# Optimization experiments

Hardware: AMD Instinct MI355X
Metric: run time of the kernel (lower is better)

The kernel has to match this reference:

```python
import jax, jax.numpy as jnp
import numpy as np
import math

D_MODEL = 2048
N_HEADS = 16
D_HEAD = D_MODEL // N_HEADS
SCALE = 1.0 / math.sqrt(D_HEAD)


def setup_inputs() -> dict:
    key = jax.random.key(0)
    kx, kq, kk, kv, ko = jax.random.split(key, 5)
    x = jax.random.normal(kx, (2, 2048, D_MODEL), dtype=jnp.float32)
    W_q = jax.random.normal(kq, (D_MODEL, D_MODEL), dtype=jnp.float32)
    W_k = jax.random.normal(kk, (D_MODEL, D_MODEL), dtype=jnp.float32)
    W_v = jax.random.normal(kv, (D_MODEL, D_MODEL), dtype=jnp.float32) * math.sqrt(2.0 / D_MODEL)
    W_o = jax.random.normal(ko, (D_MODEL, D_MODEL), dtype=jnp.float32) * math.sqrt(2.0 / D_MODEL)
    return {"x": x, "W_q": W_q, "W_k": W_k, "W_v": W_v, "W_o": W_o}


def reference(x, W_q, W_k, W_v, W_o) -> jnp.ndarray:
    B, S, D = x.shape
    q = (x @ W_q).reshape(B, S, N_HEADS, D_HEAD)  # [b, q, h, dh]
    k = (x @ W_k).reshape(B, S, N_HEADS, D_HEAD)  # [b, k, h, dh]
    v = x @ W_v                                    # [b, k, d_model] (NOT split into heads)
    scores = jnp.einsum('bqhd,bkhd->bhqk', q, k)   # [b, h, q, k]
    # Faithful quirk: additive -1e9 causal mask applied BEFORE the scale.
    mask = jnp.triu(jnp.full((S, S), -1e9, dtype=scores.dtype), k=1)
    scores = (scores + mask) * SCALE
    probs = jax.nn.softmax(scores, axis=-1)
    # Faithful quirk: sums over heads h AND keys k against full-width v.
    out = jnp.einsum('bhqk,bkd->bqd', probs, v)    # [b, q, d_model]
    return out @ W_o
```

## Files before the change

### kernel.cpp

```cpp
#include <hip/hip_runtime.h>

typedef unsigned short u16;
typedef __attribute__((ext_vector_type(8))) short bf16x8;
typedef __attribute__((ext_vector_type(4))) float f32x4;

#define DEV __device__ __forceinline__
#define EXP2(x) __builtin_amdgcn_exp2f(x)
#define LOG2(x) __builtin_amdgcn_logf(x)

DEV u16 f2bf(float f) {
  union { float f; unsigned u; } v; v.f = f;
  unsigned r = v.u + 0x7fffu + ((v.u >> 16) & 1u);
  return (u16)(r >> 16);
}
DEV float bf2f(u16 h) {
  union { unsigned u; float f; } v; v.u = ((unsigned)h) << 16;
  return v.f;
}
DEV f32x4 mfma16(bf16x8 a, bf16x8 b, f32x4 c) {
  return __builtin_amdgcn_mfma_f32_16x16x32_bf16(a, b, c, 0, 0, 0);
}
DEV void cp16(const u16* g, u16* l) {
  __builtin_amdgcn_global_load_lds((__attribute__((address_space(1))) void*)g,
                                   (__attribute__((address_space(3))) void*)l, 16, 0, 0);
}

__global__ __launch_bounds__(256) void split_pair(const float4* __restrict__ x,
                                                  u16* __restrict__ hi, u16* __restrict__ lo) {
  const size_t i = (size_t)blockIdx.x * 256 + threadIdx.x;
  const float4 v = x[i];
  ushort4 h, l;
  h.x = f2bf(v.x); l.x = f2bf(v.x - bf2f(h.x));
  h.y = f2bf(v.y); l.y = f2bf(v.y - bf2f(h.y));
  h.z = f2bf(v.z); l.z = f2bf(v.z - bf2f(h.z));
  h.w = f2bf(v.w); l.w = f2bf(v.w - bf2f(h.w));
  *(ushort4*)&hi[i * 4] = h;
  *(ushort4*)&lo[i * 4] = l;
}

template<bool LO>
__global__ __launch_bounds__(256) void transpose_split(const float* __restrict__ W,
                                                       u16* __restrict__ Th, u16* __restrict__ Tl) {
  __shared__ float t[64][65];
  const int r0 = blockIdx.y * 64, c0 = blockIdx.x * 64;
  const int rr = threadIdx.x >> 4, c4 = (threadIdx.x & 15) * 4;
#pragma unroll
  for (int p = 0; p < 4; ++p) {
    const float4 v = *(const float4*)&W[(size_t)(r0 + p * 16 + rr) * 2048 + c0 + c4];
    t[p * 16 + rr][c4 + 0] = v.x; t[p * 16 + rr][c4 + 1] = v.y;
    t[p * 16 + rr][c4 + 2] = v.z; t[p * 16 + rr][c4 + 3] = v.w;
  }
  __syncthreads();
#pragma unroll
  for (int p = 0; p < 4; ++p) {
    const int cc = p * 16 + rr;
    const float v0 = t[c4 + 0][cc], v1 = t[c4 + 1][cc], v2 = t[c4 + 2][cc], v3 = t[c4 + 3][cc];
    ushort4 h;
    h.x = f2bf(v0); h.y = f2bf(v1); h.z = f2bf(v2); h.w = f2bf(v3);
    *(ushort4*)&Th[(size_t)(c0 + cc) * 2048 + r0 + c4] = h;
    if constexpr (LO) {
      ushort4 l;
      l.x = f2bf(v0 - bf2f(h.x)); l.y = f2bf(v1 - bf2f(h.y));
      l.z = f2bf(v2 - bf2f(h.z)); l.w = f2bf(v3 - bf2f(h.w));
      *(ushort4*)&Tl[(size_t)(c0 + cc) * 2048 + r0 + c4] = l;
    }
  }
}

template<bool SPLIT3, int OUTMODE, bool KLIM>
__global__ __launch_bounds__(256, 2) void gemm_bt(
    const u16* __restrict__ Aph, const u16* __restrict__ Apl,
    const u16* __restrict__ Bph, const u16* __restrict__ Bpl,
    const u16* __restrict__ Bph2, const u16* __restrict__ Bpl2,
    void* __restrict__ C0, void* __restrict__ C1,
    void* __restrict__ C0b, void* __restrict__ C1b,
    const int M, const int N, const int K, const int bShift) {
  extern __shared__ u16 lds[];
  constexpr int T_AL = 4096;
  constexpr int T_BH = SPLIT3 ? 8192 : 4096;
  constexpr int T_BL = 12288;
  if (blockIdx.z) { Bph = Bph2; Bpl = Bpl2; C0 = C0b; C1 = C1b; }
  const int tid = threadIdx.x;
  const int wave = tid >> 6, lane = tid & 63;
  const int li = lane & 15, l4 = lane >> 4;
  const int m0 = blockIdx.y * 128, n0 = blockIdx.x * 128;
  const int wr = (wave >> 1) * 64, wc = (wave & 1) * 64;
  const u16* Bh = Bph; const u16* Bl = Bpl;
  if (bShift) { const size_t s = (size_t)(m0 >> 11) * (size_t)bShift; Bh += s; if (SPLIT3) Bl += s; }

  const f32x4 fz = {0.f, 0.f, 0.f, 0.f};
  f32x4 acc[4][4];
#pragma unroll
  for (int m = 0; m < 4; ++m)
#pragma unroll
    for (int n = 0; n < 4; ++n) acc[m][n] = fz;

  const size_t aoff = (size_t)(m0 + (tid >> 2)) * K + (tid & 3) * 8;
  const size_t boff = (size_t)(n0 + (tid >> 2)) * K + (tid & 3) * 8;
  const size_t rstep = (size_t)64 * K;
  const int s0 = tid * 8, s1 = 2048 + tid * 8;
  const int abase = (wr + li) * 32 + l4 * 8;
  const int bbase = (wc + li) * 32 + l4 * 8;
  const int kEnd = KLIM ? ((m0 & 2047) + 128 < K ? (m0 & 2047) + 128 : K) : K;

#pragma unroll 1
  for (int k0 = 0; k0 < kEnd; k0 += 32) {
    cp16(Aph + aoff + k0,         &lds[s0]);
    cp16(Aph + aoff + rstep + k0, &lds[s1]);
    cp16(Bh + boff + k0,          &lds[T_BH + s0]);
    cp16(Bh + boff + rstep + k0,  &lds[T_BH + s1]);
    if constexpr (SPLIT3) {
      cp16(Apl + aoff + k0,         &lds[T_AL + s0]);
      cp16(Apl + aoff + rstep + k0, &lds[T_AL + s1]);
      cp16(Bl + boff + k0,          &lds[T_BL + s0]);
      cp16(Bl + boff + rstep + k0,  &lds[T_BL + s1]);
    }
    __syncthreads();
    bf16x8 af[4], bf_[4];
#pragma unroll
    for (int m = 0; m < 4; ++m) af[m] = *(const bf16x8*)&lds[abase + m * 512];
#pragma unroll
    for (int n = 0; n < 4; ++n) bf_[n] = *(const bf16x8*)&lds[T_BH + bbase + n * 512];
    if constexpr (SPLIT3) {
      bf16x8 alf[4], blf[4];
#pragma unroll
      for (int m = 0; m < 4; ++m) alf[m] = *(const bf16x8*)&lds[T_AL + abase + m * 512];
#pragma unroll
      for (int n = 0; n < 4; ++n) blf[n] = *(const bf16x8*)&lds[T_BL + bbase + n * 512];
#pragma unroll
      for (int m = 0; m < 4; ++m)
#pragma unroll
        for (int n = 0; n < 4; ++n) {
          acc[m][n] = mfma16(af[m], bf_[n], acc[m][n]);
          acc[m][n] = mfma16(af[m], blf[n], acc[m][n]);
          acc[m][n] = mfma16(alf[m], bf_[n], acc[m][n]);
        }
    } else {
#pragma unroll
      for (int m = 0; m < 4; ++m)
#pragma unroll
        for (int n = 0; n < 4; ++n)
          acc[m][n] = mfma16(af[m], bf_[n], acc[m][n]);
    }
    __syncthreads();
  }

#pragma unroll
  for (int m = 0; m < 4; ++m) {
#pragma unroll
    for (int n = 0; n < 4; ++n) {
      const int rg0 = m0 + wr + m * 16 + l4 * 4;
      const int cg  = n0 + wc + n * 16 + li;
      if constexpr (OUTMODE == 0) {
        u16* Ch = (u16*)C0; u16* Cl = (u16*)C1;
#pragma unroll
        for (int r = 0; r < 4; ++r) {
          const float v = acc[m][n][r];
          const u16 h = f2bf(v);
          Ch[(size_t)(rg0 + r) * N + cg] = h;
          Cl[(size_t)(rg0 + r) * N + cg] = f2bf(v - bf2f(h));
        }
      } else if constexpr (OUTMODE == 1) {
        u16* Cs = (u16*)C0;
#pragma unroll
        for (int r = 0; r < 4; ++r) Cs[(size_t)(rg0 + r) * N + cg] = f2bf(acc[m][n][r]);
      } else if constexpr (OUTMODE == 2) {
        u16* Vt = (u16*)C0;
        ushort4 pk;
        pk.x = f2bf(acc[m][n][0]); pk.y = f2bf(acc[m][n][1]);
        pk.z = f2bf(acc[m][n][2]); pk.w = f2bf(acc[m][n][3]);
        *(ushort4*)&Vt[(size_t)(rg0 >> 11) * 4194304 + (size_t)cg * 2048 + (rg0 & 2047)] = pk;
      } else {
        float* Cf = (float*)C0;
#pragma unroll
        for (int r = 0; r < 4; ++r) Cf[(size_t)(rg0 + r) * N + cg] = acc[m][n][r];
      }
    }
  }
}

#define C2EXP 0.1275174381027786f

__global__ __launch_bounds__(256) void attn_lse_part(
    const u16* __restrict__ Qh, const u16* __restrict__ Ql,
    const u16* __restrict__ Kh, const u16* __restrict__ Kl,
    float* __restrict__ Mp, float* __restrict__ Lp) {
  const int j = blockIdx.x, qt = 15 - (int)blockIdx.y, hb = blockIdx.z;
  const int b = hb >> 4, h = hb & 15;
  const int tid = threadIdx.x;
  const int nch = (2 * qt + 5) >> 2;
  if (j >= nch) {
    if (tid < 128) {
      const size_t o = ((size_t)hb * 8 + j) * 2048 + qt * 128 + tid;
      Mp[o] = -3.0e38f; Lp[o] = 0.f;
    }
    return;
  }
  __shared__ __align__(16) u16 kb[16384];
  const int wave = tid >> 6, lane = tid & 63;
  const int li = lane & 15, l4 = lane >> 4;
  const int q0w = qt * 128 + wave * 32;
  const int rs = ((li << 6) | (l4 << 4)) ^ (((li >> 1) & 7) << 4);

  bf16x8 qfh[2][4], qfl[2][4];
#pragma unroll
  for (int mf = 0; mf < 2; ++mf) {
    const size_t qo = ((size_t)(b * 2048 + q0w + mf * 16 + li)) * 2048 + h * 128 + l4 * 8;
#pragma unroll
    for (int ks = 0; ks < 4; ++ks) {
      qfh[mf][ks] = *(const bf16x8*)&Qh[qo + ks * 32];
      qfl[mf][ks] = *(const bf16x8*)&Ql[qo + ks * 32];
    }
  }
  float m[2][4], l[2][4];
#pragma unroll
  for (int mf = 0; mf < 2; ++mf)
#pragma unroll
    for (int r = 0; r < 4; ++r) { m[mf][r] = -3.0e38f; l[mf][r] = 0.f; }

  const int kst = 4 * j;
  const int ken = min(4 * j + 4, 2 * qt + 2);
  const size_t kgbase = ((size_t)b * 2048) * 2048 + h * 128;
  const f32x4 fz = {0.f, 0.f, 0.f, 0.f};

#pragma unroll 1
  for (int t = kst; t < ken; ++t) {
    __syncthreads();
#pragma unroll
    for (int i = 0; i < 4; ++i) {
      const int o = (tid + i * 256) * 16;
      const int op = o ^ (((o >> 7) & 7) << 4);
      const int dck = op >> 12, s = (op >> 6) & 63, dl = (op >> 1) & 31;
      const size_t g = kgbase + (size_t)(t * 64 + s) * 2048 + dck * 32 + dl;
      cp16(Kh + g, kb + (o >> 1));
      cp16(Kl + g, kb + 8192 + (o >> 1));
    }
    __syncthreads();

    f32x4 av0[4], av1[4];
#pragma unroll
    for (int sn = 0; sn < 4; ++sn) {
      if (64 * t + 16 * sn <= q0w + 31) {
        f32x4 a0 = fz, a1 = fz;
#pragma unroll
        for (int ks = 0; ks < 4; ++ks) {
          const bf16x8 kh = *(const bf16x8*)((const char*)kb + ks * 4096 + (sn << 10) + rs);
          const bf16x8 kl = *(const bf16x8*)((const char*)kb + 16384 + ks * 4096 + (sn << 10) + rs);
          a0 = mfma16(qfh[0][ks], kh, a0);
          a0 = mfma16(qfh[0][ks], kl, a0);
          a0 = mfma16(qfl[0][ks], kh, a0);
          a1 = mfma16(qfh[1][ks], kh, a1);
          a1 = mfma16(qfh[1][ks], kl, a1);
          a1 = mfma16(qfl[1][ks], kh, a1);
        }
        av0[sn] = a0; av1[sn] = a1;
      }
    }
#pragma unroll
    for (int r = 0; r < 4; ++r) {
      float mx0 = m[0][r], mx1 = m[1][r];
      float am0[4], am1[4];
#pragma unroll
      for (int sn = 0; sn < 4; ++sn) {
        if (64 * t + 16 * sn <= q0w + 31) {
          const int kg = t * 64 + sn * 16 + li;
          am0[sn] = (kg <= q0w + l4 * 4 + r)      ? av0[sn][r] : -3.0e38f;
          am1[sn] = (kg <= q0w + 16 + l4 * 4 + r) ? av1[sn][r] : -3.0e38f;
          mx0 = fmaxf(mx0, am0[sn]);
          mx1 = fmaxf(mx1, am1[sn]);
        }
      }
      float s0 = 0.f, s1 = 0.f;
#pragma unroll
      for (int sn = 0; sn < 4; ++sn) {
        if (64 * t + 16 * sn <= q0w + 31) {
          s0 += EXP2((am0[sn] - mx0) * C2EXP);
          s1 += EXP2((am1[sn] - mx1) * C2EXP);
        }
      }
      l[0][r] = l[0][r] * EXP2((m[0][r] - mx0) * C2EXP) + s0;
      l[1][r] = l[1][r] * EXP2((m[1][r] - mx1) * C2EXP) + s1;
      m[0][r] = mx0; m[1][r] = mx1;
    }
  }
#pragma unroll
  for (int off = 1; off <= 8; off <<= 1) {
#pragma unroll
    for (int mf = 0; mf < 2; ++mf)
#pragma unroll
      for (int r = 0; r < 4; ++r) {
        const float om = __shfl_xor(m[mf][r], off, 64);
        const float ol = __shfl_xor(l[mf][r], off, 64);
        const float mn = fmaxf(m[mf][r], om);
        l[mf][r] = l[mf][r] * EXP2((m[mf][r] - mn) * C2EXP) + ol * EXP2((om - mn) * C2EXP);
        m[mf][r] = mn;
      }
  }
  if (li == 0) {
#pragma unroll
    for (int mf = 0; mf < 2; ++mf)
#pragma unroll
      for (int r = 0; r < 4; ++r) {
        const size_t o = ((size_t)hb * 8 + j) * 2048 + q0w + mf * 16 + l4 * 4 + r;
        Mp[o] = m[mf][r];
        Lp[o] = l[mf][r];
      }
  }
}

__global__ __launch_bounds__(256) void attn_lse_merge(
    const float* __restrict__ Mp, const float* __restrict__ Lp, float* __restrict__ LSE) {
  const int id = blockIdx.x * 256 + threadIdx.x;
  const int q = id & 2047, hb = id >> 11;
  const size_t base = (size_t)hb * 8 * 2048 + q;
  float m = Mp[base], l = Lp[base];
#pragma unroll
  for (int jj = 1; jj < 8; ++jj) {
    const float om = Mp[base + jj * 2048];
    const float ol = Lp[base + jj * 2048];
    const float mn = fmaxf(m, om);
    l = l * EXP2((m - mn) * C2EXP) + ol * EXP2((om - mn) * C2EXP);
    m = mn;
  }
  LSE[(size_t)hb * 2048 + q] = m * C2EXP + LOG2(l);
}

__global__ __launch_bounds__(256) void attn_psum(
    const u16* __restrict__ Qh, const u16* __restrict__ Ql,
    const u16* __restrict__ Kh, const u16* __restrict__ Kl,
    const float* __restrict__ LSE, u16* __restrict__ Psum) {
  const int kt = blockIdx.x, qt = blockIdx.y, b = blockIdx.z;
  const int q0 = qt * 128, k0 = kt * 64;
  const int tid = threadIdx.x;

  if (k0 > q0 + 127) {
    const size_t o = ((size_t)(b * 2048 + q0 + (tid >> 1))) * 2048 + k0 + (tid & 1) * 32;
    const uint4 z = {0u, 0u, 0u, 0u};
#pragma unroll
    for (int j2 = 0; j2 < 4; ++j2) *(uint4*)&Psum[o + j2 * 8] = z;
    return;
  }

  __shared__ __align__(16) u16 kb[16384];
  const int wave = tid >> 6, lane = tid & 63;
  const int li = lane & 15, l4 = lane >> 4;
  const int q0w = q0 + wave * 32;
  const int rs = ((li << 6) | (l4 << 4)) ^ (((li >> 1) & 7) << 4);
  int snmax = ((q0w + 31 - k0) >> 4) + 1;
  snmax = snmax < 0 ? 0 : (snmax > 4 ? 4 : snmax);

  const f32x4 fz = {0.f, 0.f, 0.f, 0.f};
  f32x4 ps[2][4];
#pragma unroll
  for (int mf = 0; mf < 2; ++mf)
#pragma unroll
    for (int sn = 0; sn < 4; ++sn) ps[mf][sn] = fz;

  const size_t kgbase = ((size_t)(b * 2048 + k0)) * 2048;
  const size_t qbase0 = ((size_t)(b * 2048 + q0w + li)) * 2048 + l4 * 8;
  const size_t qbase1 = qbase0 + (size_t)16 * 2048;
  const size_t lbase  = (size_t)(b * 16) * 2048 + q0w + l4 * 4;

#pragma unroll 1
  for (int h = 0; h < 16; ++h) {
    __syncthreads();
#pragma unroll
    for (int i = 0; i < 4; ++i) {
      const int o = (tid + i * 256) * 16;
      const int op = o ^ (((o >> 7) & 7) << 4);
      const int dck = op >> 12, s = (op >> 6) & 63, dl = (op >> 1) & 31;
      const size_t g = kgbase + (size_t)s * 2048 + h * 128 + dck * 32 + dl;
      cp16(Kh + g, kb + (o >> 1));
      cp16(Kl + g, kb + 8192 + (o >> 1));
    }
    bf16x8 qfh0[4], qfl0[4], qfh1[4], qfl1[4];
    float clse[2][4];
#pragma unroll
    for (int ks = 0; ks < 4; ++ks) {
      qfh0[ks] = *(const bf16x8*)&Qh[qbase0 + (size_t)h * 128 + ks * 32];
      qfl0[ks] = *(const bf16x8*)&Ql[qbase0 + (size_t)h * 128 + ks * 32];
      qfh1[ks] = *(const bf16x8*)&Qh[qbase1 + (size_t)h * 128 + ks * 32];
      qfl1[ks] = *(const bf16x8*)&Ql[qbase1 + (size_t)h * 128 + ks * 32];
    }
#pragma unroll
    for (int mf = 0; mf < 2; ++mf)
#pragma unroll
      for (int r = 0; r < 4; ++r)
        clse[mf][r] = LSE[lbase + (size_t)h * 2048 + mf * 16 + r];
    __syncthreads();

#pragma unroll
    for (int sn = 0; sn < 4; ++sn) {
      if (sn < snmax) {
        f32x4 a0 = fz, a1 = fz;
#pragma unroll
        for (int ks = 0; ks < 4; ++ks) {
          const bf16x8 kh = *(const bf16x8*)((const char*)kb + ks * 4096 + (sn << 10) + rs);
          const bf16x8 kl = *(const bf16x8*)((const char*)kb + 16384 + ks * 4096 + (sn << 10) + rs);
          a0 = mfma16(qfh0[ks], kh, a0);
          a0 = mfma16(qfh0[ks], kl, a0);
          a0 = mfma16(qfl0[ks], kh, a0);
          a1 = mfma16(qfh1[ks], kh, a1);
          a1 = mfma16(qfh1[ks], kl, a1);
          a1 = mfma16(qfl1[ks], kh, a1);
        }
        const int kg = k0 + sn * 16 + li;
#pragma unroll
        for (int r = 0; r < 4; ++r) {
          if (kg <= q0w + l4 * 4 + r)      ps[0][sn][r] += EXP2(a0[r] * C2EXP - clse[0][r]);
          if (kg <= q0w + 16 + l4 * 4 + r) ps[1][sn][r] += EXP2(a1[r] * C2EXP - clse[1][r]);
        }
      }
    }
  }

#pragma unroll
  for (int mf = 0; mf < 2; ++mf)
#pragma unroll
    for (int sn = 0; sn < 4; ++sn) {
      const size_t o0 = ((size_t)(b * 2048 + q0w + mf * 16 + l4 * 4)) * 2048 + k0 + sn * 16 + li;
#pragma unroll
      for (int r = 0; r < 4; ++r) Psum[o0 + (size_t)r * 2048] = f2bf(ps[mf][sn][r]);
    }
}

extern "C" void kernel_launch(void* const* d_in, const int* in_sizes, int n_in,
                              void* d_out, int out_size, void* d_ws, size_t ws_size,
                              hipStream_t stream) {
  (void)in_sizes; (void)n_in; (void)out_size; (void)ws_size;
  const float* x  = (const float*)d_in[0];
  const float* Wq = (const float*)d_in[1];
  const float* Wk = (const float*)d_in[2];
  const float* Wv = (const float*)d_in[3];
  const float* Wo = (const float*)d_in[4];
  u16* ws = (u16*)d_ws;
  const size_t E8 = 8388608, E4 = 4194304;
  u16* xh = ws;
  u16* xl = ws + E8;
  u16* Qh = ws + 2 * E8;
  u16* Ql = ws + 3 * E8;
  u16* Kh = ws + 4 * E8;
  u16* Kl = ws + 5 * E8;
  u16* Vt = ws + 6 * E8;
  u16* WTh = ws + 7 * E8;
  u16* WTl = ws + 7 * E8 + E4;
  u16* WTb = ws + 7 * E8 + 2 * E4;
  u16* WkTh = Vt;
  u16* WkTl = Vt + E4;
  float* LSEf = (float*)WTl;
  float* Mp   = LSEf + 65536;
  float* Lp   = Mp + 524288;
  u16* Psum = xl;
  u16* out1 = xh;

  split_pair<<<8192, 256, 0, stream>>>((const float4*)x, xh, xl);

  dim3 tg(32, 32);

  transpose_split<true ><<<tg, 256, 0, stream>>>(Wq, WTh, WTl);
  transpose_split<true ><<<tg, 256, 0, stream>>>(Wk, WkTh, WkTl);
  transpose_split<false><<<tg, 256, 0, stream>>>(Wv, WTb, nullptr);

  gemm_bt<true, 0, false><<<dim3(16, 32, 2), 256, 32768, stream>>>(
      xh, xl, WTh, WTl, WkTh, WkTl, Qh, Ql, Kh, Kl, 4096, 2048, 2048, 0);

  gemm_bt<false, 2, false><<<dim3(16, 32), 256, 16384, stream>>>(
      xh, nullptr, WTb, nullptr, nullptr, nullptr, Vt, nullptr, nullptr, nullptr,
      4096, 2048, 2048, 0);

  attn_lse_part<<<dim3(8, 16, 32), 256, 0, stream>>>(Qh, Ql, Kh, Kl, Mp, Lp);
  attn_lse_merge<<<256, 256, 0, stream>>>(Mp, Lp, LSEf);
  attn_psum<<<dim3(32, 16, 2), 256, 0, stream>>>(Qh, Ql, Kh, Kl, LSEf, Psum);

  gemm_bt<false, 1, true><<<dim3(16, 32), 256, 16384, stream>>>(
      Psum, nullptr, Vt, nullptr, nullptr, nullptr, out1, nullptr, nullptr, nullptr,
      4096, 2048, 2048, 4194304);

  transpose_split<false><<<tg, 256, 0, stream>>>(Wo, WTb, nullptr);
  gemm_bt<false, 3, false><<<dim3(16, 32), 256, 16384, stream>>>(
      out1, nullptr, WTb, nullptr, nullptr, nullptr, d_out, nullptr, nullptr, nullptr,
      4096, 2048, 2048, 0);
}
```

Baseline: 704.1 us.

## Use lazy-rescale online LSE, halve key splits, and XCD-swizzle GEMM tiles

The LSE partial kernel now updates each running max and sum element by element. It rescales only when a score exceeds the current max by a threshold, which avoids the per-tile max pass and most rescale exponentials. Key chunks per block double (8 tiles instead of 4), so partials and the merge loop shrink from 8 to 4 splits, giving fewer blocks and less partial traffic. GEMM tile indices are remapped so consecutive block IDs spread across the XCDs, which groups M tiles for L2 reuse. The threshold approach lets the unscaled sum grow large, up to about 2^8 per element, which carries some overflow and precision risk. The longer per-block chains reduce parallelism for causal rows.

```diff
diff --git a/kernel.cpp b/kernel.cpp
--- a/kernel.cpp
+++ b/kernel.cpp
@@ -83,7 +83,10 @@
   const int tid = threadIdx.x;
   const int wave = tid >> 6, lane = tid & 63;
   const int li = lane & 15, l4 = lane >> 4;
-  const int m0 = blockIdx.y * 128, n0 = blockIdx.x * 128;
+  const int lin0 = ((int)blockIdx.y << 4) | (int)blockIdx.x;
+  const int xcd = lin0 & 7, idx = lin0 >> 3;
+  const int m0 = ((xcd << 2) | (idx & 3)) * 128;
+  const int n0 = (idx >> 2) * 128;
   const int wr = (wave >> 1) * 64, wc = (wave & 1) * 64;
   const u16* Bh = Bph; const u16* Bl = Bpl;
   if (bShift) { const size_t s = (size_t)(m0 >> 11) * (size_t)bShift; Bh += s; if (SPLIT3) Bl += s; }
@@ -180,6 +183,7 @@
 }
 
 #define C2EXP 0.1275174381027786f
+#define DMTHR 62.73f
 
 __global__ __launch_bounds__(256) void attn_lse_part(
     const u16* __restrict__ Qh, const u16* __restrict__ Ql,
@@ -188,10 +192,10 @@
   const int j = blockIdx.x, qt = 15 - (int)blockIdx.y, hb = blockIdx.z;
   const int b = hb >> 4, h = hb & 15;
   const int tid = threadIdx.x;
-  const int nch = (2 * qt + 5) >> 2;
+  const int nch = (qt >> 2) + 1;
   if (j >= nch) {
     if (tid < 128) {
-      const size_t o = ((size_t)hb * 8 + j) * 2048 + qt * 128 + tid;
+      const size_t o = ((size_t)hb * 4 + j) * 2048 + qt * 128 + tid;
       Mp[o] = -3.0e38f; Lp[o] = 0.f;
     }
     return;
@@ -218,8 +222,8 @@
 #pragma unroll
     for (int r = 0; r < 4; ++r) { m[mf][r] = -3.0e38f; l[mf][r] = 0.f; }
 
-  const int kst = 4 * j;
-  const int ken = min(4 * j + 4, 2 * qt + 2);
+  const int kst = j * 8;
+  const int ken = min(j * 8 + 8, qt * 2 + 2);
   const size_t kgbase = ((size_t)b * 2048) * 2048 + h * 128;
   const f32x4 fz = {0.f, 0.f, 0.f, 0.f};
 
@@ -236,8 +240,6 @@
       cp16(Kl + g, kb + 8192 + (o >> 1));
     }
     __syncthreads();
-
-    f32x4 av0[4], av1[4];
 #pragma unroll
     for (int sn = 0; sn < 4; ++sn) {
       if (64 * t + 16 * sn <= q0w + 31) {
@@ -253,34 +255,21 @@
           a1 = mfma16(qfh[1][ks], kl, a1);
           a1 = mfma16(qfl[1][ks], kh, a1);
         }
-        av0[sn] = a0; av1[sn] = a1;
+        const int kg = t * 64 + sn * 16 + li;
+#pragma unroll
+        for (int r = 0; r < 4; ++r) {
+          if (kg <= q0w + l4 * 4 + r) {
+            const float d = a0[r] - m[0][r];
+            if (d > DMTHR) { l[0][r] = l[0][r] * EXP2(-d * C2EXP) + 1.f; m[0][r] = a0[r]; }
+            else           { l[0][r] += EXP2(d * C2EXP); }
+          }
+          if (kg <= q0w + 16 + l4 * 4 + r) {
+            const float d = a1[r] - m[1][r];
+            if (d > DMTHR) { l[1][r] = l[1][r] * EXP2(-d * C2EXP) + 1.f; m[1][r] = a1[r]; }
+            else           { l[1][r] += EXP2(d * C2EXP); }
+          }
+        }
       }
-    }
-#pragma unroll
-    for (int r = 0; r < 4; ++r) {
-      float mx0 = m[0][r], mx1 = m[1][r];
-      float am0[4], am1[4];
-#pragma unroll
-      for (int sn = 0; sn < 4; ++sn) {
-        if (64 * t + 16 * sn <= q0w + 31) {
-          const int kg = t * 64 + sn * 16 + li;
-          am0[sn] = (kg <= q0w + l4 * 4 + r)      ? av0[sn][r] : -3.0e38f;
-          am1[sn] = (kg <= q0w + 16 + l4 * 4 + r) ? av1[sn][r] : -3.0e38f;
-          mx0 = fmaxf(mx0, am0[sn]);
-          mx1 = fmaxf(mx1, am1[sn]);
-        }
-      }
-      float s0 = 0.f, s1 = 0.f;
-#pragma unroll
-      for (int sn = 0; sn < 4; ++sn) {
-        if (64 * t + 16 * sn <= q0w + 31) {
-          s0 += EXP2((am0[sn] - mx0) * C2EXP);
-          s1 += EXP2((am1[sn] - mx1) * C2EXP);
-        }
-      }
-      l[0][r] = l[0][r] * EXP2((m[0][r] - mx0) * C2EXP) + s0;
-      l[1][r] = l[1][r] * EXP2((m[1][r] - mx1) * C2EXP) + s1;
-      m[0][r] = mx0; m[1][r] = mx1;
     }
   }
 #pragma unroll
@@ -301,7 +290,7 @@
     for (int mf = 0; mf < 2; ++mf)
 #pragma unroll
       for (int r = 0; r < 4; ++r) {
-        const size_t o = ((size_t)hb * 8 + j) * 2048 + q0w + mf * 16 + l4 * 4 + r;
+        const size_t o = ((size_t)hb * 4 + j) * 2048 + q0w + mf * 16 + l4 * 4 + r;
         Mp[o] = m[mf][r];
         Lp[o] = l[mf][r];
       }
@@ -312,10 +301,10 @@
     const float* __restrict__ Mp, const float* __restrict__ Lp, float* __restrict__ LSE) {
   const int id = blockIdx.x * 256 + threadIdx.x;
   const int q = id & 2047, hb = id >> 11;
-  const size_t base = (size_t)hb * 8 * 2048 + q;
+  const size_t base = (size_t)hb * 4 * 2048 + q;
   float m = Mp[base], l = Lp[base];
 #pragma unroll
-  for (int jj = 1; jj < 8; ++jj) {
+  for (int jj = 1; jj < 4; ++jj) {
     const float om = Mp[base + jj * 2048];
     const float ol = Lp[base + jj * 2048];
     const float mn = fmaxf(m, om);
@@ -449,7 +438,7 @@
   u16* WkTl = Vt + E4;
   float* LSEf = (float*)WTl;
   float* Mp   = LSEf + 65536;
-  float* Lp   = Mp + 524288;
+  float* Lp   = Mp + 262144;
   u16* Psum = xl;
   u16* out1 = xh;
 
@@ -468,7 +457,7 @@
       xh, nullptr, WTb, nullptr, nullptr, nullptr, Vt, nullptr, nullptr, nullptr,
       4096, 2048, 2048, 0);
 
-  attn_lse_part<<<dim3(8, 16, 32), 256, 0, stream>>>(Qh, Ql, Kh, Kl, Mp, Lp);
+  attn_lse_part<<<dim3(4, 16, 32), 256, 0, stream>>>(Qh, Ql, Kh, Kl, Mp, Lp);
   attn_lse_merge<<<256, 256, 0, stream>>>(Mp, Lp, LSEf);
   attn_psum<<<dim3(32, 16, 2), 256, 0, stream>>>(Qh, Ql, Kh, Kl, LSEf, Psum);
 
```

New measurement: 665.3 us. -5.5%, faster.
